# Performance work log

Hardware: AMD Instinct MI355X
Metric: run time of the kernel (lower is better)

The kernel has to match this reference:

```python
import jax, jax.numpy as jnp
import numpy as np

N, K, D = 8192, 4096, 256


def setup_inputs() -> dict:
    key = jax.random.key(0)
    kx, kc, kw = jax.random.split(key, 3)
    x = jax.random.normal(kx, (N, D), dtype=jnp.float32)
    centers = jax.random.normal(kc, (K, D), dtype=jnp.float32)
    w = jax.random.normal(kw, (K,), dtype=jnp.float32)
    # bandwidth chosen so exp(-sigma * d2) stays in a healthy range for
    # Gaussian data where E[||x-c||^2] ~= 2*D
    sigma = jnp.asarray(1.0 / (2.0 * D), dtype=jnp.float32)
    return {"x": x, "centers": centers, "w": w, "sigma": sigma}


def reference(x, centers, w, sigma):
    # phi[n,k] = exp(-sigma * ||x_n - c_k||^2), computed via the GEMM
    x2 = jnp.sum(x * x, axis=-1, keepdims=True)          # [N,1]
    c2 = jnp.sum(centers * centers, axis=-1)             # [K]
    d2 = x2 + c2 - 2.0 * jnp.einsum('nd,kd->nk', x, centers)  # [N,K]
    d2 = jnp.maximum(d2, 0.0)  # clamp tiny negative round-off
    phi = jnp.exp(-sigma * d2)                           # [N,K]
    # (w * phi).sum(1) == phi @ w
    return jnp.einsum('nk,k->n', phi, w)                 # [N]
```

## Files before the change

### kernel.cpp

```cpp
#include <hip/hip_runtime.h>

#define NROWS 8192
#define NCENT 4096
#define DIM   256

#define AS1 __attribute__((address_space(1)))
#define AS3 __attribute__((address_space(3)))

typedef short bf16x8 __attribute__((ext_vector_type(8)));
typedef float f32x4  __attribute__((ext_vector_type(4)));

__device__ inline unsigned short f2bf(float f) {
    unsigned u = __float_as_uint(f);
    return (unsigned short)((u + 0x7fffu + ((u >> 16) & 1u)) >> 16);
}

__global__ __launch_bounds__(256) void prep_kernel(const float* __restrict__ x,
                                                   const float* __restrict__ c,
                                                   float* __restrict__ norms,
                                                   unsigned short* __restrict__ xbf,
                                                   unsigned short* __restrict__ cbf) {
    const int t = threadIdx.x, lane = t & 63;
    const int wbase = (blockIdx.x * 4 + (t >> 6)) * 4;
    #pragma unroll
    for (int rr = 0; rr < 4; ++rr) {
        const int gw = wbase + rr;
        const float* src;
        unsigned short* dst;
        if (gw < NROWS) { src = x + (size_t)gw * DIM;           dst = xbf + (size_t)gw * DIM; }
        else            { src = c + (size_t)(gw - NROWS) * DIM; dst = cbf + (size_t)(gw - NROWS) * DIM; }
        float4 v = ((const float4*)src)[lane];
        ushort4 b;
        b.x = f2bf(v.x); b.y = f2bf(v.y); b.z = f2bf(v.z); b.w = f2bf(v.w);
        ((ushort4*)dst)[lane] = b;
        float s = v.x * v.x + v.y * v.y + v.z * v.z + v.w * v.w;
        #pragma unroll
        for (int m = 32; m; m >>= 1) s += __shfl_xor(s, m);
        if (lane == 0) norms[gw] = s;
    }
}

__global__ __launch_bounds__(256) void rbf_mfma(const unsigned short* __restrict__ xbf,
                                                const unsigned short* __restrict__ cbf,
                                                const float* __restrict__ w,
                                                const float* __restrict__ sigp,
                                                const float* __restrict__ norms,
                                                float* __restrict__ out) {
    __shared__ __align__(16) short As[2][128 * 32];
    __shared__ __align__(16) short Bs[2][128 * 32];

    const int t    = threadIdx.x;
    const int wave = t >> 6, lane = t & 63;

    const int lin = blockIdx.y * 32 + blockIdx.x;
    const int xcd = lin & 7;
    const int pos = lin >> 3;
    const int byp = (xcd << 3) + (pos >> 5);
    const int bxp = pos & 31;
    const int m0  = byp * 128;
    const int n0  = bxp * 128;

    const int wy = wave >> 1, wx = wave & 1;
    const int lr = lane & 15;
    const int g  = lane >> 4;

    const int r_in = lane >> 2;
    const int c_l  = (lane & 3) ^ ((r_in >> 1) & 3);
    const unsigned short* gA0 = xbf + (size_t)(m0 + 32 * wave + r_in) * DIM + c_l * 8;
    const unsigned short* gB0 = cbf + (size_t)(n0 + 32 * wave + r_in) * DIM + c_l * 8;
    const int lbase = (32 * wave) * 32;

    int aoff[4], boff[4];
    #pragma unroll
    for (int i = 0; i < 4; ++i) {
        int r = 64 * wy + 16 * i + lr;
        aoff[i] = r * 32 + ((g ^ ((r >> 1) & 3)) * 8);
    }
    #pragma unroll
    for (int j = 0; j < 4; ++j) {
        int r = 64 * wx + 16 * j + lr;
        boff[j] = r * 32 + ((g ^ ((r >> 1) & 3)) * 8);
    }

    f32x4 acc[4][4];
    #pragma unroll
    for (int i = 0; i < 4; ++i)
        #pragma unroll
        for (int j = 0; j < 4; ++j) acc[i][j] = f32x4{0, 0, 0, 0};

    auto stage = [&](int s, int buf) {
        const int ko = s * 32;
        const unsigned short* a0 = gA0 + ko;
        const unsigned short* b0 = gB0 + ko;
        short* la = &As[buf][lbase];
        short* lb = &Bs[buf][lbase];
        __builtin_amdgcn_global_load_lds((const AS1 void*)a0,              (AS3 void*)la,         16, 0, 0);
        __builtin_amdgcn_global_load_lds((const AS1 void*)(a0 + 16 * DIM), (AS3 void*)(la + 512), 16, 0, 0);
        __builtin_amdgcn_global_load_lds((const AS1 void*)b0,              (AS3 void*)lb,         16, 0, 0);
        __builtin_amdgcn_global_load_lds((const AS1 void*)(b0 + 16 * DIM), (AS3 void*)(lb + 512), 16, 0, 0);
    };

    stage(0, 0);

    #pragma unroll
    for (int s = 0; s < 8; ++s) {
        __syncthreads();
        if (s < 7) stage(s + 1, (s + 1) & 1);

        const short* cA = As[s & 1];
        const short* cB = Bs[s & 1];
        bf16x8 a[4], b[4];
        #pragma unroll
        for (int i = 0; i < 4; ++i) a[i] = *(const bf16x8*)(cA + aoff[i]);
        #pragma unroll
        for (int j = 0; j < 4; ++j) b[j] = *(const bf16x8*)(cB + boff[j]);
        #pragma unroll
        for (int i = 0; i < 4; ++i)
            #pragma unroll
            for (int j = 0; j < 4; ++j)
                acc[i][j] = __builtin_amdgcn_mfma_f32_16x16x32_bf16(a[i], b[j], acc[i][j], 0, 0, 0);
    }

    const float sigma = sigp[0];
    float c2v[4], wv[4];
    #pragma unroll
    for (int j = 0; j < 4; ++j) {
        int n = n0 + 64 * wx + 16 * j + lr;
        c2v[j] = norms[NROWS + n];
        wv[j]  = w[n];
    }

    #pragma unroll
    for (int i = 0; i < 4; ++i) {
        const int mbase = m0 + 64 * wy + 16 * i + 4 * g;
        float4 x2v = *(const float4*)(norms + mbase);
        float rs[4] = {0.f, 0.f, 0.f, 0.f};
        #pragma unroll
        for (int j = 0; j < 4; ++j) {
            #pragma unroll
            for (int r = 0; r < 4; ++r) {
                float x2r = (r == 0) ? x2v.x : (r == 1) ? x2v.y : (r == 2) ? x2v.z : x2v.w;
                float d2 = x2r + c2v[j] - 2.0f * acc[i][j][r];
                d2 = fmaxf(d2, 0.0f);
                rs[r] += wv[j] * __expf(-sigma * d2);
            }
        }
        #pragma unroll
        for (int r = 0; r < 4; ++r) {
            rs[r] += __shfl_xor(rs[r], 1);
            rs[r] += __shfl_xor(rs[r], 2);
            rs[r] += __shfl_xor(rs[r], 4);
            rs[r] += __shfl_xor(rs[r], 8);
        }
        if (lr == 0) {
            #pragma unroll
            for (int r = 0; r < 4; ++r) atomicAdd(&out[mbase + r], rs[r]);
        }
    }
}

__global__ __launch_bounds__(256) void norms_kernel(const float* __restrict__ x,
                                                    const float* __restrict__ c,
                                                    float* __restrict__ ws) {
    int t = threadIdx.x, lane = t & 63;
    int gw = blockIdx.x * 4 + (t >> 6);
    const float* src;
    float* dst;
    if (gw < NROWS) { src = x + (size_t)gw * DIM;           dst = ws + gw; }
    else            { src = c + (size_t)(gw - NROWS) * DIM; dst = ws + gw; }
    float4 v = ((const float4*)src)[lane];
    float s = v.x * v.x + v.y * v.y + v.z * v.z + v.w * v.w;
    #pragma unroll
    for (int m = 32; m; m >>= 1) s += __shfl_xor(s, m);
    if (lane == 0) *dst = s;
}

__global__ __launch_bounds__(256) void rbf_kernel(const float* __restrict__ x,
                                                  const float* __restrict__ cent,
                                                  const float* __restrict__ w,
                                                  const float* __restrict__ sigp,
                                                  const float* __restrict__ norms,
                                                  float* __restrict__ out) {
    __shared__ __align__(16) short xs[64 * 32];
    __shared__ __align__(16) short cs[64 * 32];
    const int t = threadIdx.x;
    const int m0 = blockIdx.y * 64, n0 = blockIdx.x * 64;
    const int srow = t >> 2, seg = t & 3;
    const int pchunk = seg ^ ((srow >> 1) & 3);
    const int sidx = srow * 32 + pchunk * 8;
    const float* xg = x    + (size_t)(m0 + srow) * DIM + seg * 8;
    const float* cg = cent + (size_t)(n0 + srow) * DIM + seg * 8;
    const int lane = t & 63, wave = t >> 6;
    const int lr = lane & 15, lg = lane >> 4;
    const int arow = 16 * wave + lr;
    const int aidx = arow * 32 + ((lg ^ ((arow >> 1) & 3)) * 8);
    f32x4 acc[4] = {f32x4{0,0,0,0}, f32x4{0,0,0,0}, f32x4{0,0,0,0}, f32x4{0,0,0,0}};
    for (int k0 = 0; k0 < DIM; k0 += 32) {
        float4 f0 = *(const float4*)(xg + k0);
        float4 f1 = *(const float4*)(xg + k0 + 4);
        float4 g0 = *(const float4*)(cg + k0);
        float4 g1 = *(const float4*)(cg + k0 + 4);
        __syncthreads();
        union { unsigned short s[8]; int4 v; } ux, uc;
        ux.s[0]=f2bf(f0.x); ux.s[1]=f2bf(f0.y); ux.s[2]=f2bf(f0.z); ux.s[3]=f2bf(f0.w);
        ux.s[4]=f2bf(f1.x); ux.s[5]=f2bf(f1.y); ux.s[6]=f2bf(f1.z); ux.s[7]=f2bf(f1.w);
        uc.s[0]=f2bf(g0.x); uc.s[1]=f2bf(g0.y); uc.s[2]=f2bf(g0.z); uc.s[3]=f2bf(g0.w);
        uc.s[4]=f2bf(g1.x); uc.s[5]=f2bf(g1.y); uc.s[6]=f2bf(g1.z); uc.s[7]=f2bf(g1.w);
        *(int4*)(xs + sidx) = ux.v;
        *(int4*)(cs + sidx) = uc.v;
        __syncthreads();
        bf16x8 a = *(const bf16x8*)(xs + aidx);
        #pragma unroll
        for (int bt = 0; bt < 4; ++bt) {
            const int brow = 16 * bt + lr;
            bf16x8 b = *(const bf16x8*)(cs + brow * 32 + ((lg ^ ((brow >> 1) & 3)) * 8));
            acc[bt] = __builtin_amdgcn_mfma_f32_16x16x32_bf16(a, b, acc[bt], 0, 0, 0);
        }
    }
    const float sigma = sigp[0];
    const float* x2 = norms;
    const float* c2 = norms + NROWS;
    const int rbase = m0 + 16 * wave + lg * 4;
    float x2v[4];
    #pragma unroll
    for (int r = 0; r < 4; ++r) x2v[r] = x2[rbase + r];
    float rs[4] = {0.f, 0.f, 0.f, 0.f};
    #pragma unroll
    for (int bt = 0; bt < 4; ++bt) {
        const int col = n0 + 16 * bt + lr;
        const float c2v = c2[col];
        const float wvv = w[col];
        #pragma unroll
        for (int r = 0; r < 4; ++r) {
            float d2 = x2v[r] + c2v - 2.0f * acc[bt][r];
            d2 = fmaxf(d2, 0.0f);
            rs[r] += wvv * __expf(-sigma * d2);
        }
    }
    #pragma unroll
    for (int r = 0; r < 4; ++r) {
        rs[r] += __shfl_xor(rs[r], 1);
        rs[r] += __shfl_xor(rs[r], 2);
        rs[r] += __shfl_xor(rs[r], 4);
        rs[r] += __shfl_xor(rs[r], 8);
    }
    if (lr == 0) {
        #pragma unroll
        for (int r = 0; r < 4; ++r) atomicAdd(&out[rbase + r], rs[r]);
    }
}

extern "C" void kernel_launch(void* const* d_in, const int* in_sizes, int n_in,
                              void* d_out, int out_size, void* d_ws, size_t ws_size,
                              hipStream_t stream) {
    const float* x    = (const float*)d_in[0];
    const float* cent = (const float*)d_in[1];
    const float* w    = (const float*)d_in[2];
    const float* sig  = (const float*)d_in[3];
    float* out = (float*)d_out;

    const size_t norms_elems = NROWS + NCENT;
    const size_t xbf_off  = norms_elems * sizeof(float);
    const size_t cbf_off  = xbf_off + (size_t)NROWS * DIM * sizeof(unsigned short);
    const size_t ws_need  = cbf_off + (size_t)NCENT * DIM * sizeof(unsigned short);

    hipMemsetAsync(d_out, 0, (size_t)out_size * sizeof(float), stream);

    if (ws_size >= ws_need) {
        float* norms = (float*)d_ws;
        unsigned short* xbf = (unsigned short*)((char*)d_ws + xbf_off);
        unsigned short* cbf = (unsigned short*)((char*)d_ws + cbf_off);
        prep_kernel<<<(NROWS + NCENT) / 16, 256, 0, stream>>>(x, cent, norms, xbf, cbf);
        rbf_mfma<<<dim3(NCENT / 128, NROWS / 128), 256, 0, stream>>>(xbf, cbf, w, sig, norms, out);
    } else {
        float* norms = (float*)d_ws;
        norms_kernel<<<(NROWS + NCENT) / 4, 256, 0, stream>>>(x, cent, norms);
        rbf_kernel<<<dim3(NCENT / 64, NROWS / 64), 256, 0, stream>>>(x, cent, w, sig, norms, out);
    }
}
```

Before: 106.8 us.

## Load MFMA operands directly from global into registers, dropping LDS staging

Replaces the double-buffered LDS staging (global_load_lds plus syncthreads) with per-wave direct global loads of bf16 fragments into registers, software-prefetched one K-step ahead. The launch bounds now request three blocks per CU. The intent is to remove LDS traffic and barriers. In exchange each wave loads its A and B fragments itself, so data shared by waves in a block is fetched twice from cache. Each lane also reads 16-byte chunks strided by a full row, which is less coalesced and raises L2 traffic.

Result: slower. 150.8 us (+41.2%).

```diff
diff --git a/kernel.cpp b/kernel.cpp
--- a/kernel.cpp
+++ b/kernel.cpp
@@ -3,9 +3,6 @@
 #define NROWS 8192
 #define NCENT 4096
 #define DIM   256
-
-#define AS1 __attribute__((address_space(1)))
-#define AS3 __attribute__((address_space(3)))
 
 typedef short bf16x8 __attribute__((ext_vector_type(8)));
 typedef float f32x4  __attribute__((ext_vector_type(4)));
@@ -40,47 +37,33 @@
     }
 }
 
-__global__ __launch_bounds__(256) void rbf_mfma(const unsigned short* __restrict__ xbf,
-                                                const unsigned short* __restrict__ cbf,
-                                                const float* __restrict__ w,
-                                                const float* __restrict__ sigp,
-                                                const float* __restrict__ norms,
-                                                float* __restrict__ out) {
-    __shared__ __align__(16) short As[2][128 * 32];
-    __shared__ __align__(16) short Bs[2][128 * 32];
-
+__global__ __launch_bounds__(256, 3) void rbf_mfma(const unsigned short* __restrict__ xbf,
+                                                   const unsigned short* __restrict__ cbf,
+                                                   const float* __restrict__ w,
+                                                   const float* __restrict__ sigp,
+                                                   const float* __restrict__ norms,
+                                                   float* __restrict__ out) {
     const int t    = threadIdx.x;
     const int wave = t >> 6, lane = t & 63;
 
     const int lin = blockIdx.y * 32 + blockIdx.x;
     const int xcd = lin & 7;
     const int pos = lin >> 3;
-    const int byp = (xcd << 3) + (pos >> 5);
-    const int bxp = pos & 31;
-    const int m0  = byp * 128;
-    const int n0  = bxp * 128;
+    const int m0  = ((xcd << 3) + (pos >> 5)) * 128;
+    const int n0  = (pos & 31) * 128;
 
     const int wy = wave >> 1, wx = wave & 1;
     const int lr = lane & 15;
     const int g  = lane >> 4;
 
-    const int r_in = lane >> 2;
-    const int c_l  = (lane & 3) ^ ((r_in >> 1) & 3);
-    const unsigned short* gA0 = xbf + (size_t)(m0 + 32 * wave + r_in) * DIM + c_l * 8;
-    const unsigned short* gB0 = cbf + (size_t)(n0 + 32 * wave + r_in) * DIM + c_l * 8;
-    const int lbase = (32 * wave) * 32;
-
-    int aoff[4], boff[4];
-    #pragma unroll
-    for (int i = 0; i < 4; ++i) {
-        int r = 64 * wy + 16 * i + lr;
-        aoff[i] = r * 32 + ((g ^ ((r >> 1) & 3)) * 8);
-    }
-    #pragma unroll
-    for (int j = 0; j < 4; ++j) {
-        int r = 64 * wx + 16 * j + lr;
-        boff[j] = r * 32 + ((g ^ ((r >> 1) & 3)) * 8);
-    }
+    const unsigned short* pa[4];
+    const unsigned short* pb[4];
+    #pragma unroll
+    for (int i = 0; i < 4; ++i)
+        pa[i] = xbf + (size_t)(m0 + 64 * wy + 16 * i + lr) * DIM + g * 8;
+    #pragma unroll
+    for (int j = 0; j < 4; ++j)
+        pb[j] = cbf + (size_t)(n0 + 64 * wx + 16 * j + lr) * DIM + g * 8;
 
     f32x4 acc[4][4];
     #pragma unroll
@@ -88,37 +71,27 @@
         #pragma unroll
         for (int j = 0; j < 4; ++j) acc[i][j] = f32x4{0, 0, 0, 0};
 
-    auto stage = [&](int s, int buf) {
-        const int ko = s * 32;
-        const unsigned short* a0 = gA0 + ko;
-        const unsigned short* b0 = gB0 + ko;
-        short* la = &As[buf][lbase];
-        short* lb = &Bs[buf][lbase];
-        __builtin_amdgcn_global_load_lds((const AS1 void*)a0,              (AS3 void*)la,         16, 0, 0);
-        __builtin_amdgcn_global_load_lds((const AS1 void*)(a0 + 16 * DIM), (AS3 void*)(la + 512), 16, 0, 0);
-        __builtin_amdgcn_global_load_lds((const AS1 void*)b0,              (AS3 void*)lb,         16, 0, 0);
-        __builtin_amdgcn_global_load_lds((const AS1 void*)(b0 + 16 * DIM), (AS3 void*)(lb + 512), 16, 0, 0);
-    };
-
-    stage(0, 0);
+    bf16x8 a[4], b[4], an[4], bn[4];
+    #pragma unroll
+    for (int i = 0; i < 4; ++i) a[i] = *(const bf16x8*)(pa[i]);
+    #pragma unroll
+    for (int j = 0; j < 4; ++j) b[j] = *(const bf16x8*)(pb[j]);
 
     #pragma unroll
     for (int s = 0; s < 8; ++s) {
-        __syncthreads();
-        if (s < 7) stage(s + 1, (s + 1) & 1);
-
-        const short* cA = As[s & 1];
-        const short* cB = Bs[s & 1];
-        bf16x8 a[4], b[4];
-        #pragma unroll
-        for (int i = 0; i < 4; ++i) a[i] = *(const bf16x8*)(cA + aoff[i]);
-        #pragma unroll
-        for (int j = 0; j < 4; ++j) b[j] = *(const bf16x8*)(cB + boff[j]);
+        if (s < 7) {
+            #pragma unroll
+            for (int i = 0; i < 4; ++i) an[i] = *(const bf16x8*)(pa[i] + (s + 1) * 32);
+            #pragma unroll
+            for (int j = 0; j < 4; ++j) bn[j] = *(const bf16x8*)(pb[j] + (s + 1) * 32);
+        }
         #pragma unroll
         for (int i = 0; i < 4; ++i)
             #pragma unroll
             for (int j = 0; j < 4; ++j)
                 acc[i][j] = __builtin_amdgcn_mfma_f32_16x16x32_bf16(a[i], b[j], acc[i][j], 0, 0, 0);
+        #pragma unroll
+        for (int i = 0; i < 4; ++i) { a[i] = an[i]; b[i] = bn[i]; }
     }
 
     const float sigma = sigp[0];
```
